# Kernel tuning notes

Hardware: AMD Instinct MI355X
Metric: run time of the kernel (lower is better)

## Reference

```python
import jax, jax.numpy as jnp
import numpy as np

EPS = 1e-5
C = 64  # in_channels == feat_channels == out_channels


def _ln(x, g, b):
    m = jnp.mean(x, axis=-1, keepdims=True)
    v = jnp.mean(jnp.square(x - m), axis=-1, keepdims=True)
    return (x - m) * jax.lax.rsqrt(v + EPS) * g + b


def setup_inputs() -> dict:
    key = jax.random.key(0)
    ks = jax.random.split(key, 10)
    bs, nc, H, W = 8, 80, 256, 256
    d = {
        "feat": jax.random.normal(ks[0], (bs, C, H, W), jnp.float32),
        "head": jax.random.normal(ks[1], (bs, nc, C, 1), jnp.float32),
        "pred": jax.random.normal(ks[2], (bs, nc, H // 2, W // 2), jnp.float32),
        # linear transforms (stored [in, out], applied as x @ W + b)
        "W_pred_t": jax.random.normal(ks[3], (C, 2 * C), jnp.float32) * 0.05,
        "b_pred_t": jnp.zeros((2 * C,), jnp.float32),
        "W_head_t": jax.random.normal(ks[4], (C, 2 * C), jnp.float32) * 0.05,
        "b_head_t": jnp.zeros((2 * C,), jnp.float32),
        "W_pred_g": jax.random.normal(ks[5], (C, C), jnp.float32) * 0.05,
        "b_pred_g": jnp.zeros((C,), jnp.float32),
        "W_head_g": jax.random.normal(ks[6], (C, C), jnp.float32) * 0.05,
        "b_head_g": jnp.zeros((C,), jnp.float32),
        "W_fc": jax.random.normal(ks[7], (C, C), jnp.float32) * 0.05,
        "b_fc": jnp.zeros((C,), jnp.float32),
        # layernorm params
        "g_pin": jnp.ones((C,), jnp.float32), "be_pin": jnp.zeros((C,), jnp.float32),
        "g_hin": jnp.ones((C,), jnp.float32), "be_hin": jnp.zeros((C,), jnp.float32),
        "g_pout": jnp.ones((C,), jnp.float32), "be_pout": jnp.zeros((C,), jnp.float32),
        "g_hout": jnp.ones((C,), jnp.float32), "be_hout": jnp.zeros((C,), jnp.float32),
        "g_fc": jnp.ones((C,), jnp.float32), "be_fc": jnp.zeros((C,), jnp.float32),
    }
    return d


def reference(feat, head, pred,
              W_pred_t, b_pred_t, W_head_t, b_head_t,
              W_pred_g, b_pred_g, W_head_g, b_head_g,
              W_fc, b_fc,
              g_pin, be_pin, g_hin, be_hin,
              g_pout, be_pout, g_hout, be_hout,
              g_fc, be_fc):
    bs, nc = head.shape[:2]
    H, W = feat.shape[2], feat.shape[3]
    pred_up = jax.image.resize(pred, (bs, nc, H, W), method="bilinear")
    pred_up = jax.nn.sigmoid(pred_up)
    # head-aware feature assembly: [bs, nc, C]
    assemble = jnp.einsum("bnhw,bchw->bnc", pred_up, feat)
    a = assemble.reshape(-1, C)                      # [BN, C]
    BN = a.shape[0]
    # head: [bs, nc, C, kk] -> [BN, kk, C]
    hd = jnp.transpose(head.reshape(bs, nc, C, -1), (0, 1, 3, 2)).reshape(BN, -1, C)

    pf = a @ W_pred_t + b_pred_t                     # [BN, 2C]
    pf_in, pf_out = pf[:, :C], pf[:, C:]
    hf = hd @ W_head_t + b_head_t                    # [BN, kk, 2C]
    hf_in, hf_out = hf[..., :C], hf[..., C:]

    gate = hf_in * pf_in[:, None, :]                 # [BN, kk, C]
    head_gate = jax.nn.sigmoid(_ln(gate @ W_head_g + b_head_g, g_hin, be_hin))
    pred_gate = jax.nn.sigmoid(_ln(gate @ W_pred_g + b_pred_g, g_pin, be_pin))

    hf_out = _ln(hf_out, g_hout, be_hout)
    pf_out = _ln(pf_out, g_pout, be_pout)

    upd = pred_gate * pf_out[:, None, :] + head_gate * hf_out
    upd = jax.nn.relu(_ln(upd @ W_fc + b_fc, g_fc, be_fc))
    upd = upd.reshape(bs, nc, -1, C)
    upd = jnp.transpose(upd, (0, 1, 3, 2)).reshape(bs, nc, C, 1, 1)
    return upd
```

## Files before the change

### kernel.cpp

```cpp
#include <hip/hip_runtime.h>
#include <hip/hip_bf16.h>
#include <hip/hip_fp16.h>


using bf16x8 = __attribute__((ext_vector_type(8))) short;
using f32x4  = __attribute__((ext_vector_type(4))) float;

#define NPART 128
#define ROWS 2

#define SCHED_FENCE() __builtin_amdgcn_sched_barrier(0)
#define LGKM_BARRIER() do { \
  asm volatile("s_waitcnt lgkmcnt(0)" ::: "memory"); \
  __builtin_amdgcn_s_barrier(); } while (0)

__device__ __forceinline__ unsigned pk2(float lo, float hi) {
  union { __hip_bfloat162 h2; unsigned u; } cv;
  cv.h2 = __float22bfloat162_rn(make_float2(lo, hi));
  return cv.u;
}
__device__ __forceinline__ float sigAB(float a, float b) {
  return __builtin_amdgcn_rcpf(1.0f + __builtin_amdgcn_exp2f(-0.36067376f * a - 1.08202128f * b));
}
__device__ __forceinline__ float sigBA(float a, float b) {
  return __builtin_amdgcn_rcpf(1.0f + __builtin_amdgcn_exp2f(-1.08202128f * a - 0.36067376f * b));
}

__global__ __launch_bounds__(256) void k_assemble(
    const float* __restrict__ feat, const float* __restrict__ pred,
    __half* __restrict__ partial) {
  __shared__ __align__(16) unsigned short Pfrag[40 * 64 * 8];

  const int tid = threadIdx.x;
  const int b  = blockIdx.x >> 7;
  const int rb = blockIdx.x & 127;
  const int wid = tid >> 6, l = tid & 63;
  const int ch16 = l & 15, kg = l >> 4;
  const int c0 = wid << 4;
  const int h0 = rb * ROWS;
  const int gg = tid & 31, nb = tid >> 5;

  f32x4 acc[5] = {};
  const float* fwave = feat + (((size_t)(b * 64 + c0 + ch16)) << 16);
  const float* pbat  = pred + (((size_t)(b * 80)) << 14);

  #pragma unroll
  for (int r = 0; r < ROWS; ++r) {
    const int h = h0 + r;
    const int j = h >> 1;
    int r0, r1; float wy0, wy1;
    if ((h & 1) == 0) { r0 = (j > 0) ? j - 1 : 0; r1 = j; wy0 = 0.25f; wy1 = 0.75f; }
    else              { r0 = j; r1 = (j < 127) ? j + 1 : 127; wy0 = 0.75f; wy1 = 0.25f; }

    float4 p0[10], p1[10];
    #pragma unroll
    for (int i = 0; i < 10; ++i) {
      const float* pb = pbat + (((size_t)(nb + 8 * i)) << 14);
      p0[i] = *(const float4*)(pb + (r0 << 7) + gg * 4);
      p1[i] = *(const float4*)(pb + (r1 << 7) + gg * 4);
    }
    SCHED_FENCE();

    const float* fb = fwave + h * 256;
    float4 f[16];
    #pragma unroll
    for (int ks = 0; ks < 8; ++ks) {
      const int pw = ks * 32 + kg * 8;
      f[2 * ks]     = *(const float4*)(fb + pw);
      f[2 * ks + 1] = *(const float4*)(fb + pw + 4);
    }
    SCHED_FENCE();

    #pragma unroll
    for (int i = 0; i < 10; ++i) {
      const int n = nb + 8 * i;
      const float y0 = wy0 * p0[i].x + wy1 * p1[i].x;
      const float y1 = wy0 * p0[i].y + wy1 * p1[i].y;
      const float y2 = wy0 * p0[i].z + wy1 * p1[i].z;
      const float y3 = wy0 * p0[i].w + wy1 * p1[i].w;
      float yl = __shfl_up(y3, 1, 64);   if (gg == 0)  yl = y0;
      float yr = __shfl_down(y0, 1, 64); if (gg == 31) yr = y3;
      float P[8];
      P[0] = sigAB(yl, y0); P[1] = sigBA(y0, y1);
      P[2] = sigAB(y0, y1); P[3] = sigBA(y1, y2);
      P[4] = sigAB(y1, y2); P[5] = sigBA(y2, y3);
      P[6] = sigAB(y2, y3); P[7] = sigBA(y3, yr);
      uint4 s;
      s.x = pk2(P[0], P[1]); s.y = pk2(P[2], P[3]);
      s.z = pk2(P[4], P[5]); s.w = pk2(P[6], P[7]);
      const int ks = gg >> 2, kgw = gg & 3;
      const int slot = kgw * 16 + (((n & 15) ^ ks ^ (kgw << 1)) & 15);
      *(uint4*)&Pfrag[(((ks * 5 + (n >> 4)) * 64) + slot) * 8] = s;
    }
    LGKM_BARRIER();

    #pragma unroll
    for (int ks = 0; ks < 8; ++ks) {
      const float4 f0 = f[2 * ks], f1 = f[2 * ks + 1];
      union { uint4 u; bf16x8 v; } bu;
      bu.u.x = pk2(f0.x, f0.y); bu.u.y = pk2(f0.z, f0.w);
      bu.u.z = pk2(f1.x, f1.y); bu.u.w = pk2(f1.z, f1.w);
      const int slot = kg * 16 + ((ch16 ^ ks ^ (kg << 1)) & 15);
      #pragma unroll
      for (int m = 0; m < 5; ++m) {
        const bf16x8 af = *(const bf16x8*)&Pfrag[(((ks * 5 + m) * 64) + slot) * 8];
        acc[m] = __builtin_amdgcn_mfma_f32_16x16x32_bf16(af, bu.v, acc[m], 0, 0, 0);
      }
    }
    LGKM_BARRIER();
  }

  __half* po = partial + ((size_t)(b * NPART + rb)) * (80 * 64);
  #pragma unroll
  for (int m = 0; m < 5; ++m) {
    #pragma unroll
    for (int q = 0; q < 4; ++q) {
      const int n = m * 16 + kg * 4 + q;
      po[n * 64 + c0 + ch16] = __float2half(acc[m][q]);
    }
  }
}

__device__ __forceinline__ float wred64(float v) {
  #pragma unroll
  for (int off = 32; off > 0; off >>= 1) v += __shfl_xor(v, off, 64);
  return v;
}
__device__ __forceinline__ float lnorm(float x, const float* __restrict__ g,
                                       const float* __restrict__ be, int l) {
  const float m = wred64(x) * 0.015625f;
  const float d = x - m;
  const float var = wred64(d * d) * 0.015625f;
  return d * rsqrtf(var + 1e-5f) * g[l] + be[l];
}
__device__ __forceinline__ float sigmf(float x) {
  return __builtin_amdgcn_rcpf(1.0f + __builtin_amdgcn_exp2f(-1.44269504f * x));
}

__global__ __launch_bounds__(256) void k_head(
    const __half* __restrict__ partial, const float* __restrict__ head,
    const float* __restrict__ Wpt, const float* __restrict__ bpt,
    const float* __restrict__ Wht, const float* __restrict__ bht,
    const float* __restrict__ Wpg, const float* __restrict__ bpg,
    const float* __restrict__ Whg, const float* __restrict__ bhg,
    const float* __restrict__ Wfc, const float* __restrict__ bfc,
    const float* __restrict__ g_pin, const float* __restrict__ be_pin,
    const float* __restrict__ g_hin, const float* __restrict__ be_hin,
    const float* __restrict__ g_pout, const float* __restrict__ be_pout,
    const float* __restrict__ g_hout, const float* __restrict__ be_hout,
    const float* __restrict__ g_fc, const float* __restrict__ be_fc,
    float* __restrict__ out, int npart) {
  __shared__ float red[4][64];
  __shared__ float buf[4][64];
  const int tid = threadIdx.x, c = tid & 63, q = tid >> 6;
  const int r = blockIdx.x;
  const int b = r / 80, n = r % 80;
  const int npq = npart >> 2;

  const __half* pp = partial + ((size_t)b * npart + (size_t)q * npq) * 5120 + n * 64 + c;
  float s = 0.f;
  #pragma unroll 8
  for (int jj = 0; jj < npq; ++jj) s += __half2float(pp[(size_t)jj * 5120]);
  red[q][c] = s;
  __syncthreads();

  if (q == 0) {
    const float a_c = red[0][c] + red[1][c] + red[2][c] + red[3][c];
    buf[0][c] = a_c;
    buf[1][c] = head[(size_t)r * 64 + c];

    float pf_in = bpt[c], pf_out = bpt[64 + c];
    float hf_in = bht[c], hf_out = bht[64 + c];
    #pragma unroll 8
    for (int k = 0; k < 64; ++k) {
      const float av = buf[0][k];
      const float hv = buf[1][k];
      pf_in  += av * Wpt[k * 128 + c];
      pf_out += av * Wpt[k * 128 + 64 + c];
      hf_in  += hv * Wht[k * 128 + c];
      hf_out += hv * Wht[k * 128 + 64 + c];
    }
    buf[2][c] = hf_in * pf_in;

    float hg = bhg[c], pg = bpg[c];
    #pragma unroll 8
    for (int k = 0; k < 64; ++k) {
      const float gv = buf[2][k];
      hg += gv * Whg[k * 64 + c];
      pg += gv * Wpg[k * 64 + c];
    }
    const float head_gate = sigmf(lnorm(hg, g_hin, be_hin, c));
    const float pred_gate = sigmf(lnorm(pg, g_pin, be_pin, c));
    const float hfo = lnorm(hf_out, g_hout, be_hout, c);
    const float pfo = lnorm(pf_out, g_pout, be_pout, c);
    buf[3][c] = pred_gate * pfo + head_gate * hfo;

    float fc = bfc[c];
    #pragma unroll 8
    for (int k = 0; k < 64; ++k)
      fc += buf[3][k] * Wfc[k * 64 + c];
    float o = lnorm(fc, g_fc, be_fc, c);
    out[(size_t)r * 64 + c] = fmaxf(o, 0.f);
  }
}

extern "C" void kernel_launch(void* const* d_in, const int* in_sizes, int n_in,
                              void* d_out, int out_size, void* d_ws, size_t ws_size,
                              hipStream_t stream) {
  const float* feat   = (const float*)d_in[0];
  const float* head   = (const float*)d_in[1];
  const float* pred   = (const float*)d_in[2];
  const float* Wpt    = (const float*)d_in[3];
  const float* bpt    = (const float*)d_in[4];
  const float* Wht    = (const float*)d_in[5];
  const float* bht    = (const float*)d_in[6];
  const float* Wpg    = (const float*)d_in[7];
  const float* bpg    = (const float*)d_in[8];
  const float* Whg    = (const float*)d_in[9];
  const float* bhg    = (const float*)d_in[10];
  const float* Wfc    = (const float*)d_in[11];
  const float* bfc    = (const float*)d_in[12];
  const float* g_pin  = (const float*)d_in[13];
  const float* be_pin = (const float*)d_in[14];
  const float* g_hin  = (const float*)d_in[15];
  const float* be_hin = (const float*)d_in[16];
  const float* g_pout = (const float*)d_in[17];
  const float* be_pout= (const float*)d_in[18];
  const float* g_hout = (const float*)d_in[19];
  const float* be_hout= (const float*)d_in[20];
  const float* g_fc   = (const float*)d_in[21];
  const float* be_fc  = (const float*)d_in[22];
  float* out = (float*)d_out;
  __half* partial = (__half*)d_ws;

  hipLaunchKernelGGL(k_assemble, dim3(8 * NPART), dim3(256), 0, stream,
                     feat, pred, partial);
  hipLaunchKernelGGL(k_head, dim3(640), dim3(256), 0, stream,
                     partial, head, Wpt, bpt, Wht, bht, Wpg, bpg, Whg, bhg,
                     Wfc, bfc, g_pin, be_pin, g_hin, be_hin, g_pout, be_pout,
                     g_hout, be_hout, g_fc, be_fc, out, NPART);
}
```

Measured before the change: 65.72 us.

## Split assemble work into half-row blocks with more partials and occupancy

Adds a new assemble kernel in which each block handles half of one image row instead of two full rows, giving 4096 blocks instead of 1024. Each block upsamples and applies the sigmoid to its own slice of pred. Neighbouring values at the half boundary are fetched with shuffles plus one scalar load. The kernel declares launch bounds asking for four blocks per CU and remaps block order for locality. It is chosen when the workspace is large enough to hold 512 partials per batch, in exchange for four times more partial-sum data for the head kernel to reduce.

```diff
diff --git a/kernel.cpp b/kernel.cpp
--- a/kernel.cpp
+++ b/kernel.cpp
@@ -5,9 +5,6 @@
 
 using bf16x8 = __attribute__((ext_vector_type(8))) short;
 using f32x4  = __attribute__((ext_vector_type(4))) float;
-
-#define NPART 128
-#define ROWS 2
 
 #define SCHED_FENCE() __builtin_amdgcn_sched_barrier(0)
 #define LGKM_BARRIER() do { \
@@ -26,7 +23,96 @@
   return __builtin_amdgcn_rcpf(1.0f + __builtin_amdgcn_exp2f(-1.08202128f * a - 0.36067376f * b));
 }
 
-__global__ __launch_bounds__(256) void k_assemble(
+__global__ __launch_bounds__(256, 4) void k_assemble_half(
+    const float* __restrict__ feat, const float* __restrict__ pred,
+    __half* __restrict__ partial) {
+  __shared__ __align__(16) unsigned short Pfrag[20 * 64 * 8];
+
+  const int bid = blockIdx.x;
+  const int wg  = (bid & 7) * 512 + (bid >> 3);
+  const int half = wg & 1;
+  const int h    = (wg >> 1) & 255;
+  const int b    = wg >> 9;
+
+  const int tid = threadIdx.x;
+  const int gg = tid & 15, nbp = tid >> 4;
+  const int wid = tid >> 6, l = tid & 63;
+  const int ch16 = l & 15, kg = l >> 4, c0 = wid << 4;
+
+  const int j = h >> 1;
+  int r0, r1; float wy0, wy1;
+  if ((h & 1) == 0) { r0 = (j > 0) ? j - 1 : 0; r1 = j; wy0 = 0.25f; wy1 = 0.75f; }
+  else              { r0 = j; r1 = (j < 127) ? j + 1 : 127; wy0 = 0.75f; wy1 = 0.25f; }
+
+  const int cbase = half << 6;
+  const int csc   = 64 - half;
+  const float* pbat = pred + (((size_t)(b * 80)) << 14);
+
+  float4 p0[5], p1[5];
+  #pragma unroll
+  for (int i = 0; i < 5; ++i) {
+    const float* pb = pbat + (((size_t)(nbp + 16 * i)) << 14);
+    p0[i] = *(const float4*)(pb + (r0 << 7) + cbase + 4 * gg);
+    p1[i] = *(const float4*)(pb + (r1 << 7) + cbase + 4 * gg);
+  }
+
+  #pragma unroll
+  for (int i = 0; i < 5; ++i) {
+    const int n = nbp + 16 * i;
+    const float* pb = pbat + (((size_t)n) << 14);
+    const float sc = wy0 * pb[(r0 << 7) + csc] + wy1 * pb[(r1 << 7) + csc];
+    const float y0 = wy0 * p0[i].x + wy1 * p1[i].x;
+    const float y1 = wy0 * p0[i].y + wy1 * p1[i].y;
+    const float y2 = wy0 * p0[i].z + wy1 * p1[i].z;
+    const float y3 = wy0 * p0[i].w + wy1 * p1[i].w;
+    float yl = __shfl_up(y3, 1, 16);
+    float yr = __shfl_down(y0, 1, 16);
+    if (gg == 0)  yl = half ? sc : y0;
+    if (gg == 15) yr = half ? y3 : sc;
+    float P[8];
+    P[0] = sigAB(yl, y0); P[1] = sigBA(y0, y1);
+    P[2] = sigAB(y0, y1); P[3] = sigBA(y1, y2);
+    P[4] = sigAB(y1, y2); P[5] = sigBA(y2, y3);
+    P[6] = sigAB(y2, y3); P[7] = sigBA(y3, yr);
+    uint4 s;
+    s.x = pk2(P[0], P[1]); s.y = pk2(P[2], P[3]);
+    s.z = pk2(P[4], P[5]); s.w = pk2(P[6], P[7]);
+    const int ks = gg >> 2, kgw = gg & 3;
+    const int slot = kgw * 16 + ((nbp ^ ks ^ (kgw << 1)) & 15);
+    *(uint4*)&Pfrag[(((ks * 5 + i) * 64) + slot) * 8] = s;
+  }
+  __syncthreads();
+
+  const float* fb = feat + (((size_t)(b * 64 + c0 + ch16)) << 16) + h * 256 + (half << 7);
+  f32x4 acc[5] = {};
+  #pragma unroll
+  for (int ks = 0; ks < 4; ++ks) {
+    const int pw = ks * 32 + kg * 8;
+    const float4 f0 = *(const float4*)(fb + pw);
+    const float4 f1 = *(const float4*)(fb + pw + 4);
+    union { uint4 u; bf16x8 v; } bu;
+    bu.u.x = pk2(f0.x, f0.y); bu.u.y = pk2(f0.z, f0.w);
+    bu.u.z = pk2(f1.x, f1.y); bu.u.w = pk2(f1.z, f1.w);
+    const int slot = kg * 16 + ((ch16 ^ ks ^ (kg << 1)) & 15);
+    #pragma unroll
+    for (int m = 0; m < 5; ++m) {
+      const bf16x8 af = *(const bf16x8*)&Pfrag[(((ks * 5 + m) * 64) + slot) * 8];
+      acc[m] = __builtin_amdgcn_mfma_f32_16x16x32_bf16(af, bu.v, acc[m], 0, 0, 0);
+    }
+  }
+
+  __half* po = partial + ((size_t)(b * 512 + h * 2 + half)) * (80 * 64);
+  #pragma unroll
+  for (int m = 0; m < 5; ++m) {
+    #pragma unroll
+    for (int q = 0; q < 4; ++q) {
+      const int n = m * 16 + kg * 4 + q;
+      po[n * 64 + c0 + ch16] = __float2half(acc[m][q]);
+    }
+  }
+}
+
+__global__ __launch_bounds__(256) void k_assemble_full(
     const float* __restrict__ feat, const float* __restrict__ pred,
     __half* __restrict__ partial) {
   __shared__ __align__(16) unsigned short Pfrag[40 * 64 * 8];
@@ -37,7 +123,7 @@
   const int wid = tid >> 6, l = tid & 63;
   const int ch16 = l & 15, kg = l >> 4;
   const int c0 = wid << 4;
-  const int h0 = rb * ROWS;
+  const int h0 = rb * 2;
   const int gg = tid & 31, nb = tid >> 5;
 
   f32x4 acc[5] = {};
@@ -45,7 +131,7 @@
   const float* pbat  = pred + (((size_t)(b * 80)) << 14);
 
   #pragma unroll
-  for (int r = 0; r < ROWS; ++r) {
+  for (int r = 0; r < 2; ++r) {
     const int h = h0 + r;
     const int j = h >> 1;
     int r0, r1; float wy0, wy1;
@@ -110,7 +196,7 @@
     LGKM_BARRIER();
   }
 
-  __half* po = partial + ((size_t)(b * NPART + rb)) * (80 * 64);
+  __half* po = partial + ((size_t)(b * 128 + rb)) * (80 * 64);
   #pragma unroll
   for (int m = 0; m < 5; ++m) {
     #pragma unroll
@@ -233,10 +319,18 @@
   float* out = (float*)d_out;
   __half* partial = (__half*)d_ws;
 
-  hipLaunchKernelGGL(k_assemble, dim3(8 * NPART), dim3(256), 0, stream,
-                     feat, pred, partial);
+  const bool big = ws_size >= (size_t)8 * 512 * 5120 * 2;
+  const int npart = big ? 512 : 128;
+
+  if (big)
+    hipLaunchKernelGGL(k_assemble_half, dim3(4096), dim3(256), 0, stream,
+                       feat, pred, partial);
+  else
+    hipLaunchKernelGGL(k_assemble_full, dim3(1024), dim3(256), 0, stream,
+                       feat, pred, partial);
+
   hipLaunchKernelGGL(k_head, dim3(640), dim3(256), 0, stream,
                      partial, head, Wpt, bpt, Wht, bht, Wpg, bpg, Whg, bhg,
                      Wfc, bfc, g_pin, be_pin, g_hin, be_hin, g_pout, be_pout,
-                     g_hout, be_hout, g_fc, be_fc, out, NPART);
-}
+                     g_hout, be_hout, g_fc, be_fc, out, npart);
+}
```

Result: faster. 60.70 us (-7.6%).
